# Kernel tuning notes

Hardware: AMD Instinct MI355X
Metric: run time of the kernel (lower is better)

## Reference

```python
import jax, jax.numpy as jnp
import numpy as np

NUM_EMBEDDINGS = 768
HEAD_SIZE = 64

def setup_inputs() -> dict:
    key = jax.random.key(0)
    kx, kq, kk, kv = jax.random.split(key, 4)
    B, T, E, H = 4, 2048, NUM_EMBEDDINGS, HEAD_SIZE
    x = jax.random.normal(kx, (B, T, E), dtype=jnp.float32)
    s = 1.0 / np.sqrt(E)
    Wq = jax.random.normal(kq, (E, H), dtype=jnp.float32) * s
    Wk = jax.random.normal(kk, (E, H), dtype=jnp.float32) * s
    Wv = jax.random.normal(kv, (E, H), dtype=jnp.float32) * s
    return {"x": x, "Wq": Wq, "Wk": Wk, "Wv": Wv}

def reference(x, Wq, Wk, Wv):
    # x: [B,T,E]; Wq/Wk/Wv: [E,H]
    q = x @ Wq  # [B,T,H]
    k = x @ Wk
    v = x @ Wv
    scores = jnp.einsum('bth,bsh->bts', q, k) * (k.shape[-1] ** -0.5)  # [B,T,T]
    T = scores.shape[-1]
    # torch.tril(ones, diagonal=-1).bool(): True strictly below diagonal (t > s)
    row = jnp.arange(T)[:, None]
    col = jnp.arange(T)[None, :]
    mask = row > col  # strictly lower triangle masked to -inf
    scores = jnp.where(mask, -jnp.inf, scores)
    attn = jax.nn.softmax(scores, axis=-1)
    return attn @ v  # [B,T,H]
```

## Files before the change

kernel.cpp:

```cpp
#include <hip/hip_runtime.h>
#include <hip/hip_bf16.h>

#define T_ 2048
#define E_ 768

typedef __attribute__((ext_vector_type(8))) __bf16 bf16x8;
typedef __attribute__((ext_vector_type(8))) unsigned short ushort8;
typedef __attribute__((ext_vector_type(4))) unsigned short ushort4v;
typedef __attribute__((ext_vector_type(4))) float floatx4;

static __device__ __forceinline__ unsigned short f2bf(float f) {
    union { float f; unsigned u; } v; v.f = f;
    unsigned u = v.u;
    u += 0x7FFFu + ((u >> 16) & 1u);
    return (unsigned short)(u >> 16);
}

static __device__ __forceinline__ float bf2f(unsigned short s) {
    union { unsigned u; float f; } v; v.u = ((unsigned)s) << 16;
    return v.f;
}

__global__ __launch_bounds__(256) void prep_wT(const float* __restrict__ Wq,
                                               const float* __restrict__ Wk,
                                               const float* __restrict__ Wv,
                                               unsigned short* __restrict__ wT) {
    int w  = blockIdx.x / 12;
    int k0 = (blockIdx.x % 12) * 64;
    const float* W = (w == 0) ? Wq : (w == 1 ? Wk : Wv);
    __shared__ unsigned short sm[64][65];
    int tid = threadIdx.x;
    #pragma unroll
    for (int i = 0; i < 16; ++i) {
        int idx = tid + i * 256;
        int k = idx >> 6, n = idx & 63;
        sm[n][k] = f2bf(W[(size_t)(k0 + k) * 64 + n]);
    }
    __syncthreads();
    #pragma unroll
    for (int i = 0; i < 16; ++i) {
        int idx = tid + i * 256;
        int n = idx >> 6, k = idx & 63;
        wT[(size_t)w * (64 * 768) + (size_t)n * 768 + k0 + k] = sm[n][k];
    }
}

__global__ __launch_bounds__(256) void qkv_proj(const float* __restrict__ x,
                                                const unsigned short* __restrict__ wT,
                                                unsigned short* __restrict__ Qb,
                                                unsigned short* __restrict__ Kb,
                                                unsigned short* __restrict__ vT) {
    __shared__ unsigned short ws_[192][72];
    __shared__ unsigned short xs[16][72];

    int tid  = threadIdx.x;
    int lane = tid & 63, wv = tid >> 6;
    int lrow = lane & 15;
    int kh   = lane >> 4;
    int lk   = kh * 8;
    int t0   = blockIdx.x * 16;
    int n0   = wv * 48;

    int wr = tid >> 3;
    int wc = (tid & 7) * 8;
    int xr = tid >> 4;
    int xc = (tid & 15) * 4;

    floatx4 acc[3] = {};

    for (int k0 = 0; k0 < 768; k0 += 64) {
        #pragma unroll
        for (int c = 0; c < 6; ++c) {
            int rw = c * 32 + wr;
            *(ushort8*)&ws_[rw][wc] = *(const ushort8*)(wT + (size_t)rw * 768 + k0 + wc);
        }
        {
            float4 a = *(const float4*)(x + (size_t)(t0 + xr) * 768 + k0 + xc);
            ushort4v p;
            p[0] = f2bf(a.x); p[1] = f2bf(a.y); p[2] = f2bf(a.z); p[3] = f2bf(a.w);
            *(ushort4v*)&xs[xr][xc] = p;
        }
        __syncthreads();
        #pragma unroll
        for (int kc = 0; kc < 2; ++kc) {
            bf16x8 af = *(const bf16x8*)&xs[lrow][kc * 32 + lk];
            #pragma unroll
            for (int nf = 0; nf < 3; ++nf) {
                bf16x8 bfv = *(const bf16x8*)&ws_[n0 + nf * 16 + lrow][kc * 32 + lk];
                acc[nf] = __builtin_amdgcn_mfma_f32_16x16x32_bf16(af, bfv, acc[nf], 0, 0, 0);
            }
        }
        __syncthreads();
    }

    const float QS = 0.18033688011112042f;
    int mt = t0 + kh * 4;
    #pragma unroll
    for (int nf = 0; nf < 3; ++nf) {
        int nb   = n0 + nf * 16;
        int widx = nb >> 6;
        int col  = (nb & 63) + lrow;
        if (widx == 0) {
            #pragma unroll
            for (int rg = 0; rg < 4; ++rg)
                Qb[(size_t)(mt + rg) * 64 + col] = f2bf(acc[nf][rg] * QS);
        } else if (widx == 1) {
            #pragma unroll
            for (int rg = 0; rg < 4; ++rg)
                Kb[(size_t)(mt + rg) * 64 + col] = f2bf(acc[nf][rg]);
        } else {
            int b  = mt >> 11;
            int tl = mt & 2047;
            ushort4v pk;
            #pragma unroll
            for (int rg = 0; rg < 4; ++rg) pk[rg] = f2bf(acc[nf][rg]);
            *(ushort4v*)&vT[(size_t)(b * 64 + col) * T_ + tl] = pk;
        }
    }
}

__global__ __launch_bounds__(256) void attn_sum(const unsigned short* __restrict__ Qb,
                                                const unsigned short* __restrict__ Kb,
                                                const unsigned short* __restrict__ vT,
                                                float* __restrict__ lP,
                                                unsigned short* __restrict__ oP) {
    int c  = blockIdx.x;
    int qt = blockIdx.y;
    int b  = blockIdx.z;
    int t0 = qt * 64;
    int sBeg = t0 + c * 256;
    if (sBeg >= T_) return;
    int nt = (T_ - sBeg) >> 6; if (nt > 4) nt = 4;
    int p0 = (nt < 2) ? nt : 2;
    int p1 = nt - p0;

    __shared__ unsigned short ks[2][64][72];
    __shared__ unsigned short vts[2][64][72];
    __shared__ unsigned short ps[4][16][72];

    int tid  = threadIdx.x;
    int lane = tid & 63, wv = tid >> 6;
    int lrow = lane & 15;
    int lk   = (lane >> 4) * 8;
    int qrow4 = (lane >> 4) * 4;
    int sr = tid >> 2, sc = tid & 3;

    const size_t kRow = (size_t)(b * T_ + sBeg + sr) * 64 + sc * 16;
    const size_t vRow = (size_t)(b * 64 + sr) * T_ + sBeg + sc * 16;

    ushort8 k0a = *(const ushort8*)(Kb + kRow);
    ushort8 k0b = *(const ushort8*)(Kb + kRow + 8);
    ushort8 v0a = *(const ushort8*)(vT + vRow);
    ushort8 v0b = *(const ushort8*)(vT + vRow + 8);
    ushort8 k1a, k1b, v1a, v1b;
    if (p0 == 2) {
        k1a = *(const ushort8*)(Kb + kRow + 64 * 64);
        k1b = *(const ushort8*)(Kb + kRow + 64 * 64 + 8);
        v1a = *(const ushort8*)(vT + vRow + 64);
        v1b = *(const ushort8*)(vT + vRow + 64 + 8);
    }
    bf16x8 qf[2];
    {
        const unsigned short* qp = Qb + (size_t)(b * T_ + t0 + wv * 16 + lrow) * 64 + lk;
        qf[0] = *(const bf16x8*)(qp);
        qf[1] = *(const bf16x8*)(qp + 32);
    }

    *(ushort8*)&ks[0][sr][sc * 16]      = k0a;
    *(ushort8*)&ks[0][sr][sc * 16 + 8]  = k0b;
    *(ushort8*)&vts[0][sr][sc * 16]     = v0a;
    *(ushort8*)&vts[0][sr][sc * 16 + 8] = v0b;
    if (p0 == 2) {
        *(ushort8*)&ks[1][sr][sc * 16]      = k1a;
        *(ushort8*)&ks[1][sr][sc * 16 + 8]  = k1b;
        *(ushort8*)&vts[1][sr][sc * 16]     = v1a;
        *(ushort8*)&vts[1][sr][sc * 16 + 8] = v1b;
    }
    __syncthreads();

    ushort8 k2a, k2b, v2a, v2b, k3a, k3b, v3a, v3b;
    if (p1 >= 1) {
        k2a = *(const ushort8*)(Kb + kRow + 2 * 64 * 64);
        k2b = *(const ushort8*)(Kb + kRow + 2 * 64 * 64 + 8);
        v2a = *(const ushort8*)(vT + vRow + 128);
        v2b = *(const ushort8*)(vT + vRow + 128 + 8);
    }
    if (p1 == 2) {
        k3a = *(const ushort8*)(Kb + kRow + 3 * 64 * 64);
        k3b = *(const ushort8*)(Kb + kRow + 3 * 64 * 64 + 8);
        v3a = *(const ushort8*)(vT + vRow + 192);
        v3b = *(const ushort8*)(vT + vRow + 192 + 8);
    }

    float l_[4] = {0.f, 0.f, 0.f, 0.f};
    floatx4 of[4] = {};

    auto tilecomp = [&](int buf, bool domask) {
        floatx4 sf[4] = {};
        #pragma unroll
        for (int kc = 0; kc < 2; ++kc) {
            bf16x8 af = qf[kc];
            #pragma unroll
            for (int nf = 0; nf < 4; ++nf) {
                bf16x8 bfv = *(const bf16x8*)&ks[buf][nf * 16 + lrow][kc * 32 + lk];
                sf[nf] = __builtin_amdgcn_mfma_f32_16x16x32_bf16(af, bfv, sf[nf], 0, 0, 0);
            }
        }

        if (domask) {
            #pragma unroll
            for (int nf = 0; nf < 4; ++nf)
                #pragma unroll
                for (int rg = 0; rg < 4; ++rg) {
                    int sl = nf * 16 + lrow;
                    int ql = wv * 16 + qrow4 + rg;
                    if (sl < ql) sf[nf][rg] = -__builtin_inff();
                }
        }

        #pragma unroll
        for (int nf = 0; nf < 4; ++nf)
            #pragma unroll
            for (int rg = 0; rg < 4; ++rg) {
                float p = exp2f(sf[nf][rg]);
                l_[rg] += p;
                ps[wv][qrow4 + rg][nf * 16 + lrow] = f2bf(p);
            }

        #pragma unroll
        for (int kc = 0; kc < 2; ++kc) {
            bf16x8 pa = *(const bf16x8*)&ps[wv][lrow][kc * 32 + lk];
            #pragma unroll
            for (int hf = 0; hf < 4; ++hf) {
                bf16x8 vbv = *(const bf16x8*)&vts[buf][hf * 16 + lrow][kc * 32 + lk];
                of[hf] = __builtin_amdgcn_mfma_f32_16x16x32_bf16(pa, vbv, of[hf], 0, 0, 0);
            }
        }
    };

    tilecomp(0, c == 0);
    if (p0 == 2) tilecomp(1, false);

    if (p1 >= 1) {
        __syncthreads();
        *(ushort8*)&ks[0][sr][sc * 16]      = k2a;
        *(ushort8*)&ks[0][sr][sc * 16 + 8]  = k2b;
        *(ushort8*)&vts[0][sr][sc * 16]     = v2a;
        *(ushort8*)&vts[0][sr][sc * 16 + 8] = v2b;
        if (p1 == 2) {
            *(ushort8*)&ks[1][sr][sc * 16]      = k3a;
            *(ushort8*)&ks[1][sr][sc * 16 + 8]  = k3b;
            *(ushort8*)&vts[1][sr][sc * 16]     = v3a;
            *(ushort8*)&vts[1][sr][sc * 16 + 8] = v3b;
        }
        __syncthreads();
        tilecomp(0, false);
        if (p1 == 2) tilecomp(1, false);
    }

    int p = (b * 32 + qt) * 8 + c;
    #pragma unroll
    for (int rg = 0; rg < 4; ++rg) {
        float v = l_[rg];
        v += __shfl_xor(v, 1, 64);
        v += __shfl_xor(v, 2, 64);
        v += __shfl_xor(v, 4, 64);
        v += __shfl_xor(v, 8, 64);
        l_[rg] = v;
    }
    if (lrow == 0) {
        #pragma unroll
        for (int rg = 0; rg < 4; ++rg) {
            int row = wv * 16 + qrow4 + rg;
            lP[(size_t)p * 64 + row] = l_[rg];
        }
    }
    #pragma unroll
    for (int hf = 0; hf < 4; ++hf)
        #pragma unroll
        for (int rg = 0; rg < 4; ++rg) {
            int row = wv * 16 + qrow4 + rg;
            oP[((size_t)p * 64 + row) * 64 + hf * 16 + lrow] = f2bf(of[hf][rg]);
        }
}

__global__ __launch_bounds__(256) void combine(const float* __restrict__ lP,
                                               const unsigned short* __restrict__ oP,
                                               float* __restrict__ out) {
    int bq = blockIdx.x >> 2;
    int rq = blockIdx.x & 3;
    int qt = bq & 31;
    int b  = bq >> 5;
    int nch = (2303 - 64 * qt) >> 8;

    int tid = threadIdx.x;
    int r   = rq * 16 + (tid >> 4);
    int cb  = (tid & 15) * 4;

    float L = 0.f;
    float4 o = {0.f, 0.f, 0.f, 0.f};
    for (int cc = 0; cc < nch; ++cc) {
        size_t p = (size_t)(bq * 8 + cc);
        L += lP[p * 64 + r];
        ushort4v ov = *(const ushort4v*)&oP[(p * 64 + r) * 64 + cb];
        o.x += bf2f(ov[0]); o.y += bf2f(ov[1]); o.z += bf2f(ov[2]); o.w += bf2f(ov[3]);
    }
    float inv = 1.0f / L;
    float4 res = {o.x * inv, o.y * inv, o.z * inv, o.w * inv};
    *(float4*)&out[((size_t)(b * T_ + qt * 64 + r)) * 64 + cb] = res;
}

extern "C" void kernel_launch(void* const* d_in, const int* in_sizes, int n_in,
                              void* d_out, int out_size, void* d_ws, size_t ws_size,
                              hipStream_t stream) {
    const float* x  = (const float*)d_in[0];
    const float* Wq = (const float*)d_in[1];
    const float* Wk = (const float*)d_in[2];
    const float* Wv = (const float*)d_in[3];
    float* out = (float*)d_out;

    unsigned short* wT = (unsigned short*)d_ws;
    unsigned short* Qb = wT + 3 * 64 * 768;
    unsigned short* Kb = Qb + 8192 * 64;
    unsigned short* vT = Kb + 8192 * 64;
    float* lP = (float*)(vT + 4 * 64 * T_);
    unsigned short* oP = (unsigned short*)(lP + 128 * 8 * 64);

    prep_wT<<<36, 256, 0, stream>>>(Wq, Wk, Wv, wT);
    qkv_proj<<<512, 256, 0, stream>>>(x, wT, Qb, Kb, vT);
    attn_sum<<<dim3(8, 32, 4), 256, 0, stream>>>(Qb, Kb, vT, lP, oP);
    combine<<<512, 256, 0, stream>>>(lP, oP, out);
}
```

Before: 44.10 us.

## Fuse split-K combine into attention kernel via last-block atomic counter

Removes the separate combine kernel launch: each attention block stores its partial row sums and outputs with agent-scope atomic stores, bumps a per-query-tile counter, and the last live block reduces the partials and writes the final output. The counters are zeroed in the weight-prep kernel. Partial outputs are now fp32 rather than bf16, which doubles their traffic but drops one conversion step. The last block does the reduction serially, which adds tail work to that block.

```diff
diff --git a/kernel.cpp b/kernel.cpp
--- a/kernel.cpp
+++ b/kernel.cpp
@@ -16,20 +16,25 @@
     return (unsigned short)(u >> 16);
 }
 
-static __device__ __forceinline__ float bf2f(unsigned short s) {
-    union { unsigned u; float f; } v; v.u = ((unsigned)s) << 16;
-    return v.f;
+static __device__ __forceinline__ void st_agent_f32(float* p, float v) {
+    __hip_atomic_store(p, v, __ATOMIC_RELAXED, __HIP_MEMORY_SCOPE_AGENT);
+}
+static __device__ __forceinline__ float ld_agent_f32(const float* p) {
+    return __hip_atomic_load(p, __ATOMIC_RELAXED, __HIP_MEMORY_SCOPE_AGENT);
 }
 
 __global__ __launch_bounds__(256) void prep_wT(const float* __restrict__ Wq,
                                                const float* __restrict__ Wk,
                                                const float* __restrict__ Wv,
-                                               unsigned short* __restrict__ wT) {
-    int w  = blockIdx.x / 12;
-    int k0 = (blockIdx.x % 12) * 64;
+                                               unsigned short* __restrict__ wT,
+                                               unsigned int* __restrict__ cnt) {
+    int bid = blockIdx.x;
+    int tid = threadIdx.x;
+    if (bid == 0 && tid < 128) cnt[tid] = 0;
+    int w  = bid / 12;
+    int k0 = (bid % 12) * 64;
     const float* W = (w == 0) ? Wq : (w == 1 ? Wk : Wv);
     __shared__ unsigned short sm[64][65];
-    int tid = threadIdx.x;
     #pragma unroll
     for (int i = 0; i < 16; ++i) {
         int idx = tid + i * 256;
@@ -119,11 +124,12 @@
     }
 }
 
-__global__ __launch_bounds__(256) void attn_sum(const unsigned short* __restrict__ Qb,
-                                                const unsigned short* __restrict__ Kb,
-                                                const unsigned short* __restrict__ vT,
-                                                float* __restrict__ lP,
-                                                unsigned short* __restrict__ oP) {
+__global__ __launch_bounds__(256) void attn_fused(const unsigned short* __restrict__ Qb,
+                                                  const unsigned short* __restrict__ Kb,
+                                                  const unsigned short* __restrict__ vT,
+                                                  float* lP, float* oP,
+                                                  unsigned int* cnt,
+                                                  float* __restrict__ out) {
     int c  = blockIdx.x;
     int qt = blockIdx.y;
     int b  = blockIdx.z;
@@ -137,6 +143,7 @@
     __shared__ unsigned short ks[2][64][72];
     __shared__ unsigned short vts[2][64][72];
     __shared__ unsigned short ps[4][16][72];
+    __shared__ int isLast;
 
     int tid  = threadIdx.x;
     int lane = tid & 63, wv = tid >> 6;
@@ -258,7 +265,8 @@
         if (p1 == 2) tilecomp(1, false);
     }
 
-    int p = (b * 32 + qt) * 8 + c;
+    int bq = b * 32 + qt;
+    int p  = bq * 8 + c;
     #pragma unroll
     for (int rg = 0; rg < 4; ++rg) {
         float v = l_[rg];
@@ -272,7 +280,7 @@
         #pragma unroll
         for (int rg = 0; rg < 4; ++rg) {
             int row = wv * 16 + qrow4 + rg;
-            lP[(size_t)p * 64 + row] = l_[rg];
+            st_agent_f32(&lP[(size_t)p * 64 + row], l_[rg]);
         }
     }
     #pragma unroll
@@ -280,34 +288,39 @@
         #pragma unroll
         for (int rg = 0; rg < 4; ++rg) {
             int row = wv * 16 + qrow4 + rg;
-            oP[((size_t)p * 64 + row) * 64 + hf * 16 + lrow] = f2bf(of[hf][rg]);
-        }
-}
-
-__global__ __launch_bounds__(256) void combine(const float* __restrict__ lP,
-                                               const unsigned short* __restrict__ oP,
-                                               float* __restrict__ out) {
-    int bq = blockIdx.x >> 2;
-    int rq = blockIdx.x & 3;
-    int qt = bq & 31;
-    int b  = bq >> 5;
-    int nch = (2303 - 64 * qt) >> 8;
-
-    int tid = threadIdx.x;
-    int r   = rq * 16 + (tid >> 4);
-    int cb  = (tid & 15) * 4;
-
-    float L = 0.f;
-    float4 o = {0.f, 0.f, 0.f, 0.f};
-    for (int cc = 0; cc < nch; ++cc) {
-        size_t p = (size_t)(bq * 8 + cc);
-        L += lP[p * 64 + r];
-        ushort4v ov = *(const ushort4v*)&oP[(p * 64 + r) * 64 + cb];
-        o.x += bf2f(ov[0]); o.y += bf2f(ov[1]); o.z += bf2f(ov[2]); o.w += bf2f(ov[3]);
-    }
-    float inv = 1.0f / L;
-    float4 res = {o.x * inv, o.y * inv, o.z * inv, o.w * inv};
-    *(float4*)&out[((size_t)(b * T_ + qt * 64 + r)) * 64 + cb] = res;
+            st_agent_f32(&oP[((size_t)p * 64 + row) * 64 + hf * 16 + lrow], of[hf][rg]);
+        }
+
+    int nlive = (2303 - 64 * qt) >> 8;
+    asm volatile("s_waitcnt vmcnt(0)" ::: "memory");
+    __syncthreads();
+    if (tid == 0) {
+        unsigned old = __hip_atomic_fetch_add(&cnt[bq], 1u, __ATOMIC_RELAXED, __HIP_MEMORY_SCOPE_AGENT);
+        isLast = (old == (unsigned)(nlive - 1));
+    }
+    __syncthreads();
+    if (!isLast) return;
+
+    int r4 = tid >> 4;
+    int cb = (tid & 15) * 4;
+    #pragma unroll
+    for (int rq = 0; rq < 4; ++rq) {
+        int r = rq * 16 + r4;
+        float L = 0.f;
+        float4 o = {0.f, 0.f, 0.f, 0.f};
+        for (int cc = 0; cc < nlive; ++cc) {
+            size_t pp = (size_t)(bq * 8 + cc);
+            L += ld_agent_f32(&lP[pp * 64 + r]);
+            const float* op = &oP[(pp * 64 + r) * 64 + cb];
+            o.x += ld_agent_f32(op);
+            o.y += ld_agent_f32(op + 1);
+            o.z += ld_agent_f32(op + 2);
+            o.w += ld_agent_f32(op + 3);
+        }
+        float inv = 1.0f / L;
+        float4 res = {o.x * inv, o.y * inv, o.z * inv, o.w * inv};
+        *(float4*)&out[((size_t)(b * T_ + t0 + r)) * 64 + cb] = res;
+    }
 }
 
 extern "C" void kernel_launch(void* const* d_in, const int* in_sizes, int n_in,
@@ -324,10 +337,10 @@
     unsigned short* Kb = Qb + 8192 * 64;
     unsigned short* vT = Kb + 8192 * 64;
     float* lP = (float*)(vT + 4 * 64 * T_);
-    unsigned short* oP = (unsigned short*)(lP + 128 * 8 * 64);
-
-    prep_wT<<<36, 256, 0, stream>>>(Wq, Wk, Wv, wT);
+    float* oP = lP + 128 * 8 * 64;
+    unsigned int* cnt = (unsigned int*)(oP + (size_t)128 * 8 * 64 * 64);
+
+    prep_wT<<<36, 256, 0, stream>>>(Wq, Wk, Wv, wT, cnt);
     qkv_proj<<<512, 256, 0, stream>>>(x, wT, Qb, Kb, vT);
-    attn_sum<<<dim3(8, 32, 4), 256, 0, stream>>>(Qb, Kb, vT, lP, oP);
-    combine<<<512, 256, 0, stream>>>(lP, oP, out);
-}
+    attn_fused<<<dim3(8, 32, 4), 256, 0, stream>>>(Qb, Kb, vT, lP, oP, cnt, out);
+}
```

After: 60.33 us. 36.8% more time.

## Split attention into one block per 64-key tile, dropping in-block multi-tile loop

Applied to the files above, without the earlier changes.

Each attention block now handles a single 64x64 query/key tile rather than up to four key tiles. The grid grows from 8 to 32 chunks per query tile, and combine sums up to 32 partials per row. This raises parallelism and removes the in-block staging and syncs. In exchange it re-reads the Q fragments once per tile, writes four times as many bf16 partial outputs to workspace, and gives combine more partials to read.

```diff
diff --git a/kernel.cpp b/kernel.cpp
--- a/kernel.cpp
+++ b/kernel.cpp
@@ -119,7 +119,7 @@
     }
 }
 
-__global__ __launch_bounds__(256) void attn_sum(const unsigned short* __restrict__ Qb,
+__global__ __launch_bounds__(256) void attn_one(const unsigned short* __restrict__ Qb,
                                                 const unsigned short* __restrict__ Kb,
                                                 const unsigned short* __restrict__ vT,
                                                 float* __restrict__ lP,
@@ -128,14 +128,11 @@
     int qt = blockIdx.y;
     int b  = blockIdx.z;
     int t0 = qt * 64;
-    int sBeg = t0 + c * 256;
-    if (sBeg >= T_) return;
-    int nt = (T_ - sBeg) >> 6; if (nt > 4) nt = 4;
-    int p0 = (nt < 2) ? nt : 2;
-    int p1 = nt - p0;
-
-    __shared__ unsigned short ks[2][64][72];
-    __shared__ unsigned short vts[2][64][72];
+    int s0 = t0 + c * 64;
+    if (s0 >= T_) return;
+
+    __shared__ unsigned short ks[64][72];
+    __shared__ unsigned short vts[64][72];
     __shared__ unsigned short ps[4][16][72];
 
     int tid  = threadIdx.x;
@@ -145,120 +142,66 @@
     int qrow4 = (lane >> 4) * 4;
     int sr = tid >> 2, sc = tid & 3;
 
-    const size_t kRow = (size_t)(b * T_ + sBeg + sr) * 64 + sc * 16;
-    const size_t vRow = (size_t)(b * 64 + sr) * T_ + sBeg + sc * 16;
-
-    ushort8 k0a = *(const ushort8*)(Kb + kRow);
-    ushort8 k0b = *(const ushort8*)(Kb + kRow + 8);
-    ushort8 v0a = *(const ushort8*)(vT + vRow);
-    ushort8 v0b = *(const ushort8*)(vT + vRow + 8);
-    ushort8 k1a, k1b, v1a, v1b;
-    if (p0 == 2) {
-        k1a = *(const ushort8*)(Kb + kRow + 64 * 64);
-        k1b = *(const ushort8*)(Kb + kRow + 64 * 64 + 8);
-        v1a = *(const ushort8*)(vT + vRow + 64);
-        v1b = *(const ushort8*)(vT + vRow + 64 + 8);
-    }
+    const ushort8* kp = (const ushort8*)(Kb + (size_t)(b * T_ + s0 + sr) * 64 + sc * 16);
+    ushort8 ka = kp[0], kb = kp[1];
+    const ushort8* vp = (const ushort8*)(vT + (size_t)(b * 64 + sr) * T_ + s0 + sc * 16);
+    ushort8 va = vp[0], vb = vp[1];
     bf16x8 qf[2];
     {
         const unsigned short* qp = Qb + (size_t)(b * T_ + t0 + wv * 16 + lrow) * 64 + lk;
         qf[0] = *(const bf16x8*)(qp);
         qf[1] = *(const bf16x8*)(qp + 32);
     }
-
-    *(ushort8*)&ks[0][sr][sc * 16]      = k0a;
-    *(ushort8*)&ks[0][sr][sc * 16 + 8]  = k0b;
-    *(ushort8*)&vts[0][sr][sc * 16]     = v0a;
-    *(ushort8*)&vts[0][sr][sc * 16 + 8] = v0b;
-    if (p0 == 2) {
-        *(ushort8*)&ks[1][sr][sc * 16]      = k1a;
-        *(ushort8*)&ks[1][sr][sc * 16 + 8]  = k1b;
-        *(ushort8*)&vts[1][sr][sc * 16]     = v1a;
-        *(ushort8*)&vts[1][sr][sc * 16 + 8] = v1b;
-    }
+    *(ushort8*)&ks[sr][sc * 16]      = ka;
+    *(ushort8*)&ks[sr][sc * 16 + 8]  = kb;
+    *(ushort8*)&vts[sr][sc * 16]     = va;
+    *(ushort8*)&vts[sr][sc * 16 + 8] = vb;
     __syncthreads();
 
-    ushort8 k2a, k2b, v2a, v2b, k3a, k3b, v3a, v3b;
-    if (p1 >= 1) {
-        k2a = *(const ushort8*)(Kb + kRow + 2 * 64 * 64);
-        k2b = *(const ushort8*)(Kb + kRow + 2 * 64 * 64 + 8);
-        v2a = *(const ushort8*)(vT + vRow + 128);
-        v2b = *(const ushort8*)(vT + vRow + 128 + 8);
-    }
-    if (p1 == 2) {
-        k3a = *(const ushort8*)(Kb + kRow + 3 * 64 * 64);
-        k3b = *(const ushort8*)(Kb + kRow + 3 * 64 * 64 + 8);
-        v3a = *(const ushort8*)(vT + vRow + 192);
-        v3b = *(const ushort8*)(vT + vRow + 192 + 8);
+    floatx4 sf[4] = {};
+    #pragma unroll
+    for (int kc = 0; kc < 2; ++kc) {
+        bf16x8 af = qf[kc];
+        #pragma unroll
+        for (int nf = 0; nf < 4; ++nf) {
+            bf16x8 bfv = *(const bf16x8*)&ks[nf * 16 + lrow][kc * 32 + lk];
+            sf[nf] = __builtin_amdgcn_mfma_f32_16x16x32_bf16(af, bfv, sf[nf], 0, 0, 0);
+        }
+    }
+
+    if (c == 0) {
+        #pragma unroll
+        for (int nf = 0; nf < 4; ++nf)
+            #pragma unroll
+            for (int rg = 0; rg < 4; ++rg) {
+                int sl = nf * 16 + lrow;
+                int ql = wv * 16 + qrow4 + rg;
+                if (sl < ql) sf[nf][rg] = -__builtin_inff();
+            }
     }
 
     float l_[4] = {0.f, 0.f, 0.f, 0.f};
+    #pragma unroll
+    for (int nf = 0; nf < 4; ++nf)
+        #pragma unroll
+        for (int rg = 0; rg < 4; ++rg) {
+            float p = exp2f(sf[nf][rg]);
+            l_[rg] += p;
+            ps[wv][qrow4 + rg][nf * 16 + lrow] = f2bf(p);
+        }
+
     floatx4 of[4] = {};
-
-    auto tilecomp = [&](int buf, bool domask) {
-        floatx4 sf[4] = {};
-        #pragma unroll
-        for (int kc = 0; kc < 2; ++kc) {
-            bf16x8 af = qf[kc];
-            #pragma unroll
-            for (int nf = 0; nf < 4; ++nf) {
-                bf16x8 bfv = *(const bf16x8*)&ks[buf][nf * 16 + lrow][kc * 32 + lk];
-                sf[nf] = __builtin_amdgcn_mfma_f32_16x16x32_bf16(af, bfv, sf[nf], 0, 0, 0);
-            }
-        }
-
-        if (domask) {
-            #pragma unroll
-            for (int nf = 0; nf < 4; ++nf)
-                #pragma unroll
-                for (int rg = 0; rg < 4; ++rg) {
-                    int sl = nf * 16 + lrow;
-                    int ql = wv * 16 + qrow4 + rg;
-                    if (sl < ql) sf[nf][rg] = -__builtin_inff();
-                }
-        }
-
-        #pragma unroll
-        for (int nf = 0; nf < 4; ++nf)
-            #pragma unroll
-            for (int rg = 0; rg < 4; ++rg) {
-                float p = exp2f(sf[nf][rg]);
-                l_[rg] += p;
-                ps[wv][qrow4 + rg][nf * 16 + lrow] = f2bf(p);
-            }
-
-        #pragma unroll
-        for (int kc = 0; kc < 2; ++kc) {
-            bf16x8 pa = *(const bf16x8*)&ps[wv][lrow][kc * 32 + lk];
-            #pragma unroll
-            for (int hf = 0; hf < 4; ++hf) {
-                bf16x8 vbv = *(const bf16x8*)&vts[buf][hf * 16 + lrow][kc * 32 + lk];
-                of[hf] = __builtin_amdgcn_mfma_f32_16x16x32_bf16(pa, vbv, of[hf], 0, 0, 0);
-            }
-        }
-    };
-
-    tilecomp(0, c == 0);
-    if (p0 == 2) tilecomp(1, false);
-
-    if (p1 >= 1) {
-        __syncthreads();
-        *(ushort8*)&ks[0][sr][sc * 16]      = k2a;
-        *(ushort8*)&ks[0][sr][sc * 16 + 8]  = k2b;
-        *(ushort8*)&vts[0][sr][sc * 16]     = v2a;
-        *(ushort8*)&vts[0][sr][sc * 16 + 8] = v2b;
-        if (p1 == 2) {
-            *(ushort8*)&ks[1][sr][sc * 16]      = k3a;
-            *(ushort8*)&ks[1][sr][sc * 16 + 8]  = k3b;
-            *(ushort8*)&vts[1][sr][sc * 16]     = v3a;
-            *(ushort8*)&vts[1][sr][sc * 16 + 8] = v3b;
-        }
-        __syncthreads();
-        tilecomp(0, false);
-        if (p1 == 2) tilecomp(1, false);
-    }
-
-    int p = (b * 32 + qt) * 8 + c;
+    #pragma unroll
+    for (int kc = 0; kc < 2; ++kc) {
+        bf16x8 pa = *(const bf16x8*)&ps[wv][lrow][kc * 32 + lk];
+        #pragma unroll
+        for (int hf = 0; hf < 4; ++hf) {
+            bf16x8 vbv = *(const bf16x8*)&vts[hf * 16 + lrow][kc * 32 + lk];
+            of[hf] = __builtin_amdgcn_mfma_f32_16x16x32_bf16(pa, vbv, of[hf], 0, 0, 0);
+        }
+    }
+
+    int p = ((b * 32 + qt) << 5) + c;
     #pragma unroll
     for (int rg = 0; rg < 4; ++rg) {
         float v = l_[rg];
@@ -291,7 +234,7 @@
     int rq = blockIdx.x & 3;
     int qt = bq & 31;
     int b  = bq >> 5;
-    int nch = (2303 - 64 * qt) >> 8;
+    int nch = 32 - qt;
 
     int tid = threadIdx.x;
     int r   = rq * 16 + (tid >> 4);
@@ -300,7 +243,7 @@
     float L = 0.f;
     float4 o = {0.f, 0.f, 0.f, 0.f};
     for (int cc = 0; cc < nch; ++cc) {
-        size_t p = (size_t)(bq * 8 + cc);
+        size_t p = (size_t)((bq << 5) + cc);
         L += lP[p * 64 + r];
         ushort4v ov = *(const ushort4v*)&oP[(p * 64 + r) * 64 + cb];
         o.x += bf2f(ov[0]); o.y += bf2f(ov[1]); o.z += bf2f(ov[2]); o.w += bf2f(ov[3]);
@@ -324,10 +267,10 @@
     unsigned short* Kb = Qb + 8192 * 64;
     unsigned short* vT = Kb + 8192 * 64;
     float* lP = (float*)(vT + 4 * 64 * T_);
-    unsigned short* oP = (unsigned short*)(lP + 128 * 8 * 64);
+    unsigned short* oP = (unsigned short*)(lP + 128 * 32 * 64);
 
     prep_wT<<<36, 256, 0, stream>>>(Wq, Wk, Wv, wT);
     qkv_proj<<<512, 256, 0, stream>>>(x, wT, Qb, Kb, vT);
-    attn_sum<<<dim3(8, 32, 4), 256, 0, stream>>>(Qb, Kb, vT, lP, oP);
+    attn_one<<<dim3(32, 32, 4), 256, 0, stream>>>(Qb, Kb, vT, lP, oP);
     combine<<<512, 256, 0, stream>>>(lP, oP, out);
 }
```

After: 48.65 us. 1.1x slower.
